# Optimization experiments

Measured on AMD Instinct MI355X. Metric: run time of the kernel, lower is better.

## Reference

```python
import jax, jax.numpy as jnp
import numpy as np
from jax import lax

EPS = 1e-5

def bn(x, g, b):
    # training-mode BatchNorm2d over (N, H, W)
    m = jnp.mean(x, axis=(0, 2, 3), keepdims=True)
    v = jnp.var(x, axis=(0, 2, 3), keepdims=True)
    return (x - m) * lax.rsqrt(v + EPS) * g[None, :, None, None] + b[None, :, None, None]

def conv1x1(x, W):
    # x: [b,c,h,w], W: [o,c]
    return jnp.einsum('bchw,oc->bohw', x, W)

def conv3x3(x, W):
    # W: [o,i,3,3]
    return lax.conv_general_dilated(x, W, (1, 1), 'SAME',
                                    dimension_numbers=('NCHW', 'OIHW', 'NCHW'))

def lga(x, Wqkv, Wproj, g, b):
    # LinearGlobalAttention: O(N) global attention
    bsz, c, h, w = x.shape
    qkv = conv1x1(x, Wqkv)                       # [b, 3c, h, w]
    q, k, v = jnp.split(qkv, 3, axis=1)
    q = q.reshape(bsz, c, h * w)                 # [b, c, N]
    k = jax.nn.softmax(k.reshape(bsz, c, h * w), axis=-1)
    v = v.reshape(bsz, c, h * w)
    ctx = jnp.einsum('bcn,bdn->bcd', k, v)       # [b, c, c]
    out = jnp.einsum('bcd,bcn->bdn', ctx, q)     # context^T @ q -> [b, c, N]
    out = out.reshape(bsz, c, h, w)
    return jax.nn.relu(bn(conv1x1(out, Wproj), g, b))


def setup_inputs() -> dict:
    key = jax.random.key(0)
    ks = jax.random.split(key, 12)
    B, Cin, Cout, H, W = 16, 128, 256, 64, 64
    wd = Cout // 4  # branch width = 64
    sc = 0.05
    inp = {
        'x': jax.random.normal(ks[0], (B, Cin, H, W), jnp.float32),
        'W_sc': jax.random.normal(ks[1], (Cout, Cin), jnp.float32) * sc,
        'g_sc': jnp.ones((Cout,), jnp.float32),
        'b_sc': jnp.zeros((Cout,), jnp.float32),
        'W1': jax.random.normal(ks[2], (Cout, Cin), jnp.float32) * sc,
        'g1': jnp.ones((Cout,), jnp.float32),
        'b1': jnp.zeros((Cout,), jnp.float32),
        'Wb0': jax.random.normal(ks[3], (wd, wd), jnp.float32) * sc,
        'gb0': jnp.ones((wd,), jnp.float32),
        'bb0': jnp.zeros((wd,), jnp.float32),
        'Wb1': jax.random.normal(ks[4], (wd, wd, 3, 3), jnp.float32) * sc,
        'gb1': jnp.ones((wd,), jnp.float32),
        'bb1': jnp.zeros((wd,), jnp.float32),
        'Wqkv2': jax.random.normal(ks[5], (3 * wd, wd), jnp.float32) * sc,
        'Wproj2': jax.random.normal(ks[6], (wd, wd), jnp.float32) * sc,
        'ga2': jnp.ones((wd,), jnp.float32),
        'ba2': jnp.zeros((wd,), jnp.float32),
        'Wqkv3': jax.random.normal(ks[7], (3 * wd, wd), jnp.float32) * sc,
        'Wproj3': jax.random.normal(ks[8], (wd, wd), jnp.float32) * sc,
        'ga3': jnp.ones((wd,), jnp.float32),
        'ba3': jnp.zeros((wd,), jnp.float32),
        'W2': jax.random.normal(ks[9], (Cout, Cout), jnp.float32) * sc,
        'g2': jnp.ones((Cout,), jnp.float32),
        'b2': jnp.zeros((Cout,), jnp.float32),
    }
    return inp


def reference(x, W_sc, g_sc, b_sc, W1, g1, b1,
              Wb0, gb0, bb0, Wb1, gb1, bb1,
              Wqkv2, Wproj2, ga2, ba2,
              Wqkv3, Wproj3, ga3, ba3,
              W2, g2, b2):
    residual = bn(conv1x1(x, W_sc), g_sc, b_sc)
    h = jax.nn.relu(bn(conv1x1(x, W1), g1, b1))      # [b, 256, H, W]
    s0, s1, s2, s3 = jnp.split(h, 4, axis=1)          # width = 64 each
    o0 = jax.nn.relu(bn(conv1x1(s0, Wb0), gb0, bb0))  # k=1 branch
    o1 = jax.nn.relu(bn(conv3x3(s1, Wb1), gb1, bb1))  # k=3 branch
    o2 = lga(s2, Wqkv2, Wproj2, ga2, ba2)             # k=5 -> attention
    o3 = lga(s3, Wqkv3, Wproj3, ga3, ba3)             # k=7 -> attention
    out = jnp.concatenate([o0, o1, o2, o3], axis=1)
    out = bn(conv1x1(out, W2), g2, b2) + residual
    return jax.nn.relu(out)
```

## Files before the change

### kernel.cpp

```cpp
#include <hip/hip_runtime.h>
#include <hip/hip_bf16.h>

using bf16 = __hip_bfloat16;
typedef __bf16 bf16v8 __attribute__((ext_vector_type(8)));
typedef float f32x4 __attribute__((ext_vector_type(4)));

#define HW 4096
#define ROWS 65536
#define BRSTRIDE 4194304

#define AS1 const __attribute__((address_space(1))) void*
#define AS3 __attribute__((address_space(3))) void*

__global__ void r4_cvt_w(const float* __restrict__ Wsc, const float* __restrict__ W1,
                         const float* __restrict__ Wb0,
                         const float* __restrict__ Wqkv2, const float* __restrict__ Wqkv3,
                         const float* __restrict__ W2, const float* __restrict__ Wb1,
                         bf16* __restrict__ wbase, bf16* __restrict__ wp,
                         float* __restrict__ stats) {
    int i = blockIdx.x * 256 + threadIdx.x;
    if (i < 2048) stats[i] = 0.f;
    if (i < 159744) {
        const float* s; int off;
        if      (i < 32768)  { s = Wsc;   off = i; }
        else if (i < 65536)  { s = W1;    off = i - 32768; }
        else if (i < 69632)  { s = Wb0;   off = i - 65536; }
        else if (i < 81920)  { s = Wqkv2; off = i - 69632; }
        else if (i < 94208)  { s = Wqkv3; off = i - 81920; }
        else                 { s = W2;    off = i - 94208; }
        wbase[i] = __float2bfloat16(s[off]);
    } else {
        int k = i - 159744;
        int tap = k / 4096, rem = k % 4096;
        int o = rem >> 6, c = rem & 63;
        wp[k] = __float2bfloat16(Wb1[(size_t)(o * 64 + c) * 9 + tap]);
    }
}

__global__ void r4_cvt_x(const float* __restrict__ x, bf16* __restrict__ xT) {
    __shared__ bf16 tile[64 * 65];
    int b = blockIdx.z, c0 = blockIdx.y * 64, n0 = blockIdx.x * 64;
    int t = threadIdx.x;
#pragma unroll
    for (int i = 0; i < 4; i++) {
        int idx = i * 256 + t;
        int cc = idx >> 4, n4 = (idx & 15) * 4;
        float4 v = *(const float4*)&x[((size_t)(b * 128 + c0 + cc)) * HW + n0 + n4];
        tile[(n4 + 0) * 65 + cc] = __float2bfloat16(v.x);
        tile[(n4 + 1) * 65 + cc] = __float2bfloat16(v.y);
        tile[(n4 + 2) * 65 + cc] = __float2bfloat16(v.z);
        tile[(n4 + 3) * 65 + cc] = __float2bfloat16(v.w);
    }
    __syncthreads();
#pragma unroll
    for (int i = 0; i < 2; i++) {
        int u = i * 256 + t;
        int nn = u >> 3, p = u & 7;
        bf16v8 v;
#pragma unroll
        for (int j = 0; j < 8; j++) v[j] = (__bf16)tile[nn * 65 + p * 8 + j];
        *(bf16v8*)&xT[((size_t)(b * HW + n0 + nn)) * 128 + c0 + p * 8] = v;
    }
}

template <int KK>
__global__ __launch_bounds__(256) void ga_gemm(
        const bf16* __restrict__ A, int a_stride,
        const bf16* __restrict__ W, int w_stride,
        bf16* __restrict__ out0, bf16* __restrict__ out1, int split,
        int out_stride,
        float* __restrict__ stat0, float* __restrict__ stat1,
        int scol0, int scol1,
        const float* __restrict__ tsums,
        const float* __restrict__ tg0, const float* __restrict__ tb0,
        const float* __restrict__ tg1, const float* __restrict__ tb1,
        const float* __restrict__ tg2, const float* __restrict__ tb2,
        const float* __restrict__ tg3, const float* __restrict__ tb3) {
    __shared__ bf16 shmem[2 * 128 * 128];
    __shared__ float sredS[256], sredQ[256];
    __shared__ float scS[256], shS[256];
    bf16* As = shmem;
    bf16* Ws = shmem + 16384;

    int t = threadIdx.x;
    int wave = t >> 6, lane = t & 63;
    int lo = lane & 15, quad = lane >> 4;
    int wr = wave >> 1, wc = wave & 1;
    int b = blockIdx.z;
    long grow = (long)b * HW + blockIdx.x * 128;
    int o0 = blockIdx.y * 128;
    const bf16* Wb = W + (long)o0 * w_stride;

    if (tsums) {
        int qi = t >> 6, ci = t & 63;
        const float* gp = qi == 0 ? tg0 : qi == 1 ? tg1 : qi == 2 ? tg2 : tg3;
        const float* bp = qi == 0 ? tb0 : qi == 1 ? tb1 : qi == 2 ? tb2 : tb3;
        float mean = tsums[t] * (1.f / 65536.f);
        float var  = tsums[256 + t] * (1.f / 65536.f) - mean * mean;
        float s = gp[ci] * rsqrtf(var + 1e-5f);
        scS[t] = s; shS[t] = bp[ci] - mean * s;
    }

    f32x4 acc[4][4];
#pragma unroll
    for (int m = 0; m < 4; m++)
#pragma unroll
        for (int n = 0; n < 4; n++) acc[m][n] = (f32x4){0.f, 0.f, 0.f, 0.f};

#pragma unroll
    for (int ph = 0; ph < KK / 128; ph++) {
        int k0 = ph * 128;
#pragma unroll
        for (int j = 0; j < 8; j++) {
            int i = j * 4 + wave;
            int ci = i * 64 + lane;
            int R = ci >> 4, cc = ci & 15;
            int sw = ((cc ^ (R & 7)) << 3);
            __builtin_amdgcn_global_load_lds(
                (AS1)(A + (grow + R) * (long)a_stride + k0 + sw),
                (AS3)(As + i * 512), 16, 0, 0);
            __builtin_amdgcn_global_load_lds(
                (AS1)(Wb + (long)R * w_stride + k0 + sw),
                (AS3)(Ws + i * 512), 16, 0, 0);
        }
        asm volatile("s_waitcnt vmcnt(0)" ::: "memory");
        __syncthreads();
        if (tsums) {
#pragma unroll
            for (int i = 0; i < 8; i++) {
                int ci = i * 256 + t;
                int R = ci >> 4, p = ci & 15;
                int chb = k0 + ((p ^ (R & 7)) << 3);
                bf16v8 v = *(const bf16v8*)&As[R * 128 + p * 8];
#pragma unroll
                for (int j = 0; j < 8; j++) {
                    float f = (float)v[j] * scS[chb + j] + shS[chb + j];
                    v[j] = (__bf16)fmaxf(f, 0.f);
                }
                *(bf16v8*)&As[R * 128 + p * 8] = v;
            }
            __syncthreads();
        }
#pragma unroll
        for (int ks = 0; ks < 128; ks += 32) {
            int kk = (ks >> 3) + quad;
            bf16v8 av[4], wv[4];
#pragma unroll
            for (int m = 0; m < 4; m++) {
                int R = wr * 64 + m * 16 + lo;
                av[m] = *(const bf16v8*)&As[R * 128 + ((kk ^ (R & 7)) << 3)];
            }
#pragma unroll
            for (int n = 0; n < 4; n++) {
                int R = wc * 64 + n * 16 + lo;
                wv[n] = *(const bf16v8*)&Ws[R * 128 + ((kk ^ (R & 7)) << 3)];
            }
#pragma unroll
            for (int m = 0; m < 4; m++)
#pragma unroll
                for (int n = 0; n < 4; n++)
                    acc[m][n] = __builtin_amdgcn_mfma_f32_16x16x32_bf16(av[m], wv[n], acc[m][n], 0, 0, 0);
        }
        __syncthreads();
    }

    bf16* Ot = shmem;
#pragma unroll
    for (int m = 0; m < 4; m++)
#pragma unroll
        for (int n = 0; n < 4; n++)
#pragma unroll
            for (int r = 0; r < 4; r++)
                Ot[(wr * 64 + m * 16 + quad * 4 + r) * 136 + wc * 64 + n * 16 + lo] =
                    __float2bfloat16(acc[m][n][r]);
    __syncthreads();
    bool low = o0 < split;
    bf16* op = low ? out0 : out1;
    int oc0 = low ? o0 : o0 - split;
#pragma unroll
    for (int i = 0; i < 8; i++) {
        int u = i * 256 + t;
        int lr = u >> 4, cg = u & 15;
        *(bf16v8*)&op[(grow + lr) * (long)out_stride + oc0 + cg * 8] =
            *(const bf16v8*)&Ot[lr * 136 + cg * 8];
    }
    if (stat0) {
        int c = t & 127, half = t >> 7;
        float s = 0.f, q = 0.f;
#pragma unroll
        for (int r = 0; r < 64; r++) {
            float v = __bfloat162float(Ot[(half * 64 + r) * 136 + c]);
            s += v; q += v * v;
        }
        sredS[t] = s; sredQ[t] = q;
        __syncthreads();
        if (t < 128) {
            float ss = sredS[t] + sredS[t + 128];
            float qq = sredQ[t] + sredQ[t + 128];
            float* st = low ? stat0 : stat1;
            int ci = (low ? scol0 + o0 : scol1 + o0 - split) + c;
            atomicAdd(&st[ci], ss);
            atomicAdd(&st[256 + ci], qq);
        }
    }
}

__global__ __launch_bounds__(256) void gq_gemm(
        const bf16* __restrict__ y1,
        const bf16* __restrict__ wq2, const bf16* __restrict__ wq3,
        const bf16* __restrict__ wb0,
        bf16* __restrict__ qs, bf16* __restrict__ ks, bf16* __restrict__ vs,
        bf16* __restrict__ obuf, float* __restrict__ stats,
        const float* __restrict__ asums,
        const float* __restrict__ g1, const float* __restrict__ b1) {
    __shared__ bf16 shmem[256 * 64 + 64 * 64];
    __shared__ float sredS[256], sredQ[256];
    __shared__ float scS[64], shS[64];
    bf16* As = shmem;
    bf16* Ws = shmem + 256 * 64;

    int t = threadIdx.x;
    int wave = t >> 6, lane = t & 63;
    int lo = lane & 15, quad = lane >> 4;
    int b = blockIdx.z, y = blockIdx.y;
    long grow = (long)b * HW + blockIdx.x * 256;

    const bf16* Ab; const bf16* Wb; bf16* outp; int ostride; float* st; int col0;
    if (y == 6) {
        Ab = y1; Wb = wb0; outp = obuf; ostride = 256; st = stats; col0 = 0;
    } else {
        int br = y / 3, sel = y - br * 3;
        col0 = 128 + br * 64;
        Ab = y1 + col0;
        Wb = (br ? wq3 : wq2) + sel * 4096;
        outp = (sel == 0 ? qs : sel == 1 ? ks : vs) + (long)br * BRSTRIDE;
        ostride = 64; st = nullptr;
    }
    if (t < 64) {
        int ch = col0 + t;
        float mean = asums[ch] * (1.f / 65536.f);
        float var  = asums[256 + ch] * (1.f / 65536.f) - mean * mean;
        float s = g1[ch] * rsqrtf(var + 1e-5f);
        scS[t] = s; shS[t] = b1[ch] - mean * s;
    }

    f32x4 acc[4][4];
#pragma unroll
    for (int m = 0; m < 4; m++)
#pragma unroll
        for (int n = 0; n < 4; n++) acc[m][n] = (f32x4){0.f, 0.f, 0.f, 0.f};

#pragma unroll
    for (int j = 0; j < 8; j++) {
        int ci = (j * 4 + wave) * 64 + lane;
        int R = ci >> 3, cc = ci & 7;
        __builtin_amdgcn_global_load_lds(
            (AS1)(Ab + (grow + R) * 256L + ((cc ^ (R & 7)) << 3)),
            (AS3)(As + (j * 4 + wave) * 512), 16, 0, 0);
    }
#pragma unroll
    for (int j = 0; j < 2; j++) {
        int ci = (j * 4 + wave) * 64 + lane;
        int R = ci >> 3, cc = ci & 7;
        __builtin_amdgcn_global_load_lds(
            (AS1)(Wb + R * 64 + ((cc ^ (R & 7)) << 3)),
            (AS3)(Ws + (j * 4 + wave) * 512), 16, 0, 0);
    }
    asm volatile("s_waitcnt vmcnt(0)" ::: "memory");
    __syncthreads();
#pragma unroll
    for (int i = 0; i < 8; i++) {
        int ci = i * 256 + t;
        int R = ci >> 3, p = ci & 7;
        int chb = (p ^ (R & 7)) << 3;
        bf16v8 v = *(const bf16v8*)&As[R * 64 + p * 8];
#pragma unroll
        for (int j = 0; j < 8; j++) {
            float f = (float)v[j] * scS[chb + j] + shS[chb + j];
            v[j] = (__bf16)fmaxf(f, 0.f);
        }
        *(bf16v8*)&As[R * 64 + p * 8] = v;
    }
    __syncthreads();

#pragma unroll
    for (int ks_ = 0; ks_ < 64; ks_ += 32) {
        bf16v8 av[4], wv[4];
#pragma unroll
        for (int m = 0; m < 4; m++) {
            int R = wave * 64 + m * 16 + lo;
            av[m] = *(const bf16v8*)&As[R * 64 + ((((ks_ >> 3) + quad) ^ (R & 7)) << 3)];
        }
#pragma unroll
        for (int n = 0; n < 4; n++) {
            int o = n * 16 + lo;
            wv[n] = *(const bf16v8*)&Ws[o * 64 + ((((ks_ >> 3) + quad) ^ (o & 7)) << 3)];
        }
#pragma unroll
        for (int m = 0; m < 4; m++)
#pragma unroll
            for (int n = 0; n < 4; n++)
                acc[m][n] = __builtin_amdgcn_mfma_f32_16x16x32_bf16(av[m], wv[n], acc[m][n], 0, 0, 0);
    }
    __syncthreads();

    bf16* Ot = shmem;
#pragma unroll
    for (int m = 0; m < 4; m++)
#pragma unroll
        for (int n = 0; n < 4; n++)
#pragma unroll
            for (int r = 0; r < 4; r++)
                Ot[(wave * 64 + m * 16 + quad * 4 + r) * 72 + n * 16 + lo] =
                    __float2bfloat16(acc[m][n][r]);
    __syncthreads();
#pragma unroll
    for (int i = 0; i < 8; i++) {
        int u = i * 256 + t;
        int lr = u >> 3, cg = u & 7;
        *(bf16v8*)&outp[(grow + lr) * (long)ostride + cg * 8] =
            *(const bf16v8*)&Ot[lr * 72 + cg * 8];
    }
    if (st) {
        int c = t & 63, qtr = t >> 6;
        float s = 0.f, q = 0.f;
#pragma unroll
        for (int r = 0; r < 64; r++) {
            float v = __bfloat162float(Ot[(qtr * 64 + r) * 72 + c]);
            s += v; q += v * v;
        }
        sredS[t] = s; sredQ[t] = q;
        __syncthreads();
        if (t < 64) {
            float ss = sredS[t] + sredS[t + 64] + sredS[t + 128] + sredS[t + 192];
            float qq = sredQ[t] + sredQ[t + 64] + sredQ[t + 128] + sredQ[t + 192];
            atomicAdd(&st[t], ss);
            atomicAdd(&st[256 + t], qq);
        }
    }
}

__global__ __launch_bounds__(256) void gp_gemm(
        const bf16* __restrict__ qs, const bf16* __restrict__ M,
        bf16* __restrict__ obuf, float* __restrict__ stats) {
    __shared__ bf16 shmem[256 * 64 + 64 * 64];
    __shared__ float sredS[256], sredQ[256];
    bf16* As = shmem;
    bf16* Ws = shmem + 256 * 64;

    int t = threadIdx.x;
    int wave = t >> 6, lane = t & 63;
    int lo = lane & 15, quad = lane >> 4;
    int b = blockIdx.z, y = blockIdx.y;
    long grow = (long)b * HW + blockIdx.x * 256;
    const bf16* Ab = qs + (long)y * BRSTRIDE;
    const bf16* Wb = M + y * 65536 + (long)b * 4096;
    int oc0 = 128 + y * 64;

    f32x4 acc[4][4];
#pragma unroll
    for (int m = 0; m < 4; m++)
#pragma unroll
        for (int n = 0; n < 4; n++) acc[m][n] = (f32x4){0.f, 0.f, 0.f, 0.f};

#pragma unroll
    for (int j = 0; j < 8; j++) {
        int ci = (j * 4 + wave) * 64 + lane;
        int R = ci >> 3, cc = ci & 7;
        __builtin_amdgcn_global_load_lds(
            (AS1)(Ab + (grow + R) * 64L + ((cc ^ (R & 7)) << 3)),
            (AS3)(As + (j * 4 + wave) * 512), 16, 0, 0);
    }
#pragma unroll
    for (int j = 0; j < 2; j++) {
        int ci = (j * 4 + wave) * 64 + lane;
        int R = ci >> 3, cc = ci & 7;
        __builtin_amdgcn_global_load_lds(
            (AS1)(Wb + R * 64 + ((cc ^ (R & 7)) << 3)),
            (AS3)(Ws + (j * 4 + wave) * 512), 16, 0, 0);
    }
    asm volatile("s_waitcnt vmcnt(0)" ::: "memory");
    __syncthreads();

#pragma unroll
    for (int ks_ = 0; ks_ < 64; ks_ += 32) {
        bf16v8 av[4], wv[4];
#pragma unroll
        for (int m = 0; m < 4; m++) {
            int R = wave * 64 + m * 16 + lo;
            av[m] = *(const bf16v8*)&As[R * 64 + ((((ks_ >> 3) + quad) ^ (R & 7)) << 3)];
        }
#pragma unroll
        for (int n = 0; n < 4; n++) {
            int o = n * 16 + lo;
            wv[n] = *(const bf16v8*)&Ws[o * 64 + ((((ks_ >> 3) + quad) ^ (o & 7)) << 3)];
        }
#pragma unroll
        for (int m = 0; m < 4; m++)
#pragma unroll
            for (int n = 0; n < 4; n++)
                acc[m][n] = __builtin_amdgcn_mfma_f32_16x16x32_bf16(av[m], wv[n], acc[m][n], 0, 0, 0);
    }
    __syncthreads();

    bf16* Ot = shmem;
#pragma unroll
    for (int m = 0; m < 4; m++)
#pragma unroll
        for (int n = 0; n < 4; n++)
#pragma unroll
            for (int r = 0; r < 4; r++)
                Ot[(wave * 64 + m * 16 + quad * 4 + r) * 72 + n * 16 + lo] =
                    __float2bfloat16(acc[m][n][r]);
    __syncthreads();
#pragma unroll
    for (int i = 0; i < 8; i++) {
        int u = i * 256 + t;
        int lr = u >> 3, cg = u & 7;
        *(bf16v8*)&obuf[(grow + lr) * 256L + oc0 + cg * 8] =
            *(const bf16v8*)&Ot[lr * 72 + cg * 8];
    }
    {
        int c = t & 63, qtr = t >> 6;
        float s = 0.f, q = 0.f;
#pragma unroll
        for (int r = 0; r < 64; r++) {
            float v = __bfloat162float(Ot[(qtr * 64 + r) * 72 + c]);
            s += v; q += v * v;
        }
        sredS[t] = s; sredQ[t] = q;
        __syncthreads();
        if (t < 64) {
            float ss = sredS[t] + sredS[t + 64] + sredS[t + 128] + sredS[t + 192];
            float qq = sredQ[t] + sredQ[t + 64] + sredQ[t + 128] + sredQ[t + 192];
            atomicAdd(&stats[oc0 + t], ss);
            atomicAdd(&stats[256 + oc0 + t], qq);
        }
    }
}

__global__ __launch_bounds__(256) void r12_conv3(
        const bf16* __restrict__ hT, const bf16* __restrict__ wp,
        bf16* __restrict__ obuf, float* __restrict__ stat,
        const float* __restrict__ asums,
        const float* __restrict__ g1, const float* __restrict__ b1) {
    __shared__ bf16 As[6 * 66 * 64];
    __shared__ bf16 Wt[9 * 64 * 64];
    __shared__ float sredS[256], sredQ[256];
    __shared__ float scS[64], shS[64];

    int t = threadIdx.x;
    int wave = t >> 6, lane = t & 63;
    int lo = lane & 15, quad = lane >> 4;
    int b = blockIdx.y, y0 = blockIdx.x * 4;

    if (t < 64) {
        int ch = 64 + t;
        float mean = asums[ch] * (1.f / 65536.f);
        float var  = asums[256 + ch] * (1.f / 65536.f) - mean * mean;
        float s = g1[ch] * rsqrtf(var + 1e-5f);
        scS[t] = s; shS[t] = b1[ch] - mean * s;
    }

#pragma unroll
    for (int j = 0; j < 18; j++) {
        int i = j * 4 + wave;
        int ci = i * 64 + lane;
        int tap = ci >> 9, rem = ci & 511, o = rem >> 3, ck = rem & 7;
        __builtin_amdgcn_global_load_lds(
            (AS1)(wp + tap * 4096 + o * 64 + ((ck ^ (o & 7)) << 3)),
            (AS3)(Wt + i * 512), 16, 0, 0);
    }
#pragma unroll
    for (int j = 0; j < 12; j++) {
        int i = j * 4 + wave;
        int row = i >> 3, seg = i & 7;
        int yy = y0 - 1 + row;
        if (yy >= 0 && yy < 64) {
            int xg = seg * 8 + (lane >> 3), ck = lane & 7;
            __builtin_amdgcn_global_load_lds(
                (AS1)(hT + ((long)b * HW + yy * 64 + xg) * 256 + 64 + ((ck ^ (xg & 7)) << 3)),
                (AS3)(As + row * 4224 + 64 + seg * 512), 16, 0, 0);
        } else {
            *(bf16v8*)&As[row * 4224 + 64 + seg * 512 + lane * 8] = (bf16v8){0,0,0,0,0,0,0,0};
        }
    }
    if (t < 96) {
        int yr = t >> 4, side = (t >> 3) & 1, ck = t & 7;
        *(bf16v8*)&As[yr * 4224 + (side ? 65 : 0) * 64 + ck * 8] = (bf16v8){0,0,0,0,0,0,0,0};
    }
    asm volatile("s_waitcnt vmcnt(0)" ::: "memory");
    __syncthreads();
#pragma unroll
    for (int i = 0; i < 12; i++) {
        int ci = i * 256 + t;
        int row = ci >> 9, rem = ci & 511;
        int xg = rem >> 3, p = rem & 7;
        int yy = y0 - 1 + row;
        if (yy >= 0 && yy < 64) {
            int chb = (p ^ (xg & 7)) << 3;
            bf16v8 v = *(const bf16v8*)&As[row * 4224 + (xg + 1) * 64 + p * 8];
#pragma unroll
            for (int j = 0; j < 8; j++) {
                float f = (float)v[j] * scS[chb + j] + shS[chb + j];
                v[j] = (__bf16)fmaxf(f, 0.f);
            }
            *(bf16v8*)&As[row * 4224 + (xg + 1) * 64 + p * 8] = v;
        }
    }
    __syncthreads();

    f32x4 acc[4][4];
#pragma unroll
    for (int m = 0; m < 4; m++)
#pragma unroll
        for (int n = 0; n < 4; n++) acc[m][n] = (f32x4){0.f, 0.f, 0.f, 0.f};

#pragma unroll
    for (int tap = 0; tap < 9; tap++) {
        int dy = tap / 3 - 1, dx = tap % 3 - 1;
        int yr = wave + 1 + dy;
#pragma unroll
        for (int ks8 = 0; ks8 < 8; ks8 += 4) {
            int kk = ks8 + quad;
            bf16v8 wv[4];
#pragma unroll
            for (int ot = 0; ot < 4; ot++) {
                int o = ot * 16 + lo;
                wv[ot] = *(const bf16v8*)&Wt[tap * 4096 + o * 64 + ((kk ^ (o & 7)) << 3)];
            }
#pragma unroll
            for (int m = 0; m < 4; m++) {
                int xp = m * 16 + lo + dx;
                bf16v8 av = *(const bf16v8*)&As[yr * 4224 + (xp + 1) * 64 + ((kk ^ (xp & 7)) << 3)];
#pragma unroll
                for (int ot = 0; ot < 4; ot++)
                    acc[m][ot] = __builtin_amdgcn_mfma_f32_16x16x32_bf16(av, wv[ot], acc[m][ot], 0, 0, 0);
            }
        }
    }
    __syncthreads();

    bf16* Ot = As;
#pragma unroll
    for (int m = 0; m < 4; m++)
#pragma unroll
        for (int ot = 0; ot < 4; ot++)
#pragma unroll
            for (int r = 0; r < 4; r++)
                Ot[(wave * 64 + m * 16 + quad * 4 + r) * 72 + ot * 16 + lo] =
                    __float2bfloat16(acc[m][ot][r]);
    __syncthreads();

    long grow = (long)b * HW + y0 * 64;
#pragma unroll
    for (int i = 0; i < 8; i++) {
        int u = i * 256 + t;
        int lr = u >> 3, cg = u & 7;
        *(bf16v8*)&obuf[(grow + lr) * 256 + 64 + cg * 8] = *(const bf16v8*)&Ot[lr * 72 + cg * 8];
    }
    {
        int c = t & 63, qtr = t >> 6;
        float s = 0.f, q = 0.f;
#pragma unroll
        for (int r = 0; r < 64; r++) {
            float v = __bfloat162float(Ot[(qtr * 64 + r) * 72 + c]);
            s += v; q += v * v;
        }
        sredS[t] = s; sredQ[t] = q;
        __syncthreads();
        if (t < 64) {
            float ss = sredS[t] + sredS[t + 64] + sredS[t + 128] + sredS[t + 192];
            float qq = sredQ[t] + sredQ[t + 64] + sredQ[t + 128] + sredQ[t + 192];
            atomicAdd(&stat[64 + t], ss);
            atomicAdd(&stat[256 + 64 + t], qq);
        }
    }
}

__global__ __launch_bounds__(256) void r14_softctx(
        const bf16* __restrict__ ks_t, const bf16* __restrict__ vs_t,
        float* __restrict__ ctx_p, float* __restrict__ lpart) {
    __shared__ bf16 Ks[64 * 136];
    __shared__ bf16 Vs[64 * 136];
    __shared__ float red[32 * 64];
    int t = threadIdx.x;
    int wave = t >> 6, lane = t & 63;
    int lo = lane & 15, quad = lane >> 4;
    int b = blockIdx.y, bx = blockIdx.x, z = blockIdx.z;
    const bf16* kb = ks_t + (long)z * BRSTRIDE;
    const bf16* vb = vs_t + (long)z * BRSTRIDE;

    f32x4 acc[4];
#pragma unroll
    for (int ot = 0; ot < 4; ot++) acc[ot] = (f32x4){0.f, 0.f, 0.f, 0.f};
    float sm[8];
#pragma unroll
    for (int j = 0; j < 8; j++) sm[j] = 0.f;

    for (int it = 0; it < 2; it++) {
        long n0 = ((long)bx * 2 + it) * 128;
        __syncthreads();
#pragma unroll
        for (int sub = 0; sub < 4; sub++) {
            int r = sub * 32 + (t >> 3), cg = t & 7;
            long row = (long)b * HW + n0 + r;
            bf16v8 k8 = *(const bf16v8*)(kb + row * 64 + cg * 8);
            bf16v8 v8 = *(const bf16v8*)(vb + row * 64 + cg * 8);
#pragma unroll
            for (int j = 0; j < 8; j++) {
                int c = cg * 8 + j;
                float e = expf((float)k8[j]);
                sm[j] += e;
                Ks[c * 136 + r] = __float2bfloat16(e);
                Vs[c * 136 + r] = (bf16)v8[j];
            }
        }
        __syncthreads();
#pragma unroll
        for (int ks = 0; ks < 128; ks += 32) {
            bf16v8 av = *(const bf16v8*)&Ks[(wave * 16 + lo) * 136 + ks + quad * 8];
#pragma unroll
            for (int ot = 0; ot < 4; ot++) {
                bf16v8 bv = *(const bf16v8*)&Vs[(ot * 16 + lo) * 136 + ks + quad * 8];
                acc[ot] = __builtin_amdgcn_mfma_f32_16x16x32_bf16(av, bv, acc[ot], 0, 0, 0);
            }
        }
    }
    long blk = ((long)z * 16 + b) * 16 + bx;
#pragma unroll
    for (int ot = 0; ot < 4; ot++) {
#pragma unroll
        for (int r = 0; r < 4; r++) {
            int c = wave * 16 + quad * 4 + r;
            int d = ot * 16 + lo;
            ctx_p[(blk * 64 + c) * 64 + d] = acc[ot][r];
        }
    }
    {
        int rg = t >> 3, cg = t & 7;
#pragma unroll
        for (int j = 0; j < 8; j++) red[rg * 64 + cg * 8 + j] = sm[j];
        __syncthreads();
        if (t < 64) {
            float s = 0.f;
#pragma unroll
            for (int i = 0; i < 32; i++) s += red[i * 64 + t];
            lpart[blk * 64 + t] = s;
        }
    }
}

__global__ __launch_bounds__(256) void r15_mproj(
        const float* __restrict__ Wp2, const float* __restrict__ Wp3,
        const float* __restrict__ ctx_p, const float* __restrict__ lpart,
        bf16* __restrict__ M) {
    __shared__ float ctxS[16 * 68];
    __shared__ float ilS[16];
    int b = blockIdx.x, qq = blockIdx.y, z = blockIdx.z, t = threadIdx.x;
    int e = t & 63, cg = t >> 6;
    const float* Wp = z ? Wp3 : Wp2;
    long zb = (long)z * 16 + b;
#pragma unroll
    for (int i = 0; i < 4; i++) {
        int u = i * 256 + t;
        int c_l = u >> 6, d = u & 63;
        float s = 0.f;
#pragma unroll
        for (int p = 0; p < 16; p++)
            s += ctx_p[((zb * 16 + p) * 64 + qq * 16 + c_l) * 64 + d];
        ctxS[c_l * 68 + d] = s;
    }
    if (t < 16) {
        float l = 0.f;
#pragma unroll
        for (int p = 0; p < 16; p++)
            l += lpart[(zb * 16 + p) * 64 + qq * 16 + t];
        ilS[t] = 1.f / l;
    }
    float wreg[64];
#pragma unroll
    for (int i = 0; i < 16; i++) {
        float4 v = *(const float4*)&Wp[e * 64 + i * 4];
        wreg[i * 4 + 0] = v.x; wreg[i * 4 + 1] = v.y;
        wreg[i * 4 + 2] = v.z; wreg[i * 4 + 3] = v.w;
    }
    __syncthreads();
#pragma unroll
    for (int ci = 0; ci < 4; ci++) {
        int c_l = cg * 4 + ci;
        float a = 0.f;
#pragma unroll
        for (int dg = 0; dg < 16; dg++) {
            float4 cv = *(const float4*)&ctxS[c_l * 68 + dg * 4];
            a += wreg[dg * 4 + 0] * cv.x + wreg[dg * 4 + 1] * cv.y
               + wreg[dg * 4 + 2] * cv.z + wreg[dg * 4 + 3] * cv.w;
        }
        M[(long)z * 65536 + (long)b * 4096 + e * 64 + qq * 16 + c_l] =
            __float2bfloat16(a * ilS[c_l]);
    }
}

__global__ void r6_final(const bf16* __restrict__ y2, const bf16* __restrict__ ysc,
                         const float* __restrict__ s2sums, const float* __restrict__ scsums,
                         const float* __restrict__ g2, const float* __restrict__ b2,
                         const float* __restrict__ gsc, const float* __restrict__ bsc,
                         float* __restrict__ out) {
    __shared__ float lo_[64 * 65];
    __shared__ float sc2[64], sh2[64], scc[64], shc[64];
    int b = blockIdx.z, c0 = blockIdx.y * 64, n0 = blockIdx.x * 64;
    int t = threadIdx.x;
    if (t < 64) {
        int ch = c0 + t;
        float m2 = s2sums[ch] * (1.f / 65536.f);
        float v2 = s2sums[256 + ch] * (1.f / 65536.f) - m2 * m2;
        float s = g2[ch] * rsqrtf(v2 + 1e-5f);
        sc2[t] = s; sh2[t] = b2[ch] - m2 * s;
        float mc = scsums[ch] * (1.f / 65536.f);
        float vc = scsums[256 + ch] * (1.f / 65536.f) - mc * mc;
        float s2_ = gsc[ch] * rsqrtf(vc + 1e-5f);
        scc[t] = s2_; shc[t] = bsc[ch] - mc * s2_;
    }
    __syncthreads();
    for (int half = 0; half < 2; half++) {
        int r = half * 32 + (t >> 3), cc = (t & 7) * 8;
        long row = (long)b * HW + n0 + r;
        bf16v8 a8 = *(const bf16v8*)&y2[row * 256 + c0 + cc];
        bf16v8 s8 = *(const bf16v8*)&ysc[row * 256 + c0 + cc];
#pragma unroll
        for (int j = 0; j < 8; j++) {
            int c = cc + j;
            float v = (float)a8[j] * sc2[c] + sh2[c] + (float)s8[j] * scc[c] + shc[c];
            lo_[c * 65 + r] = fmaxf(v, 0.f);
        }
    }
    __syncthreads();
#pragma unroll
    for (int i = 0; i < 4; i++) {
        int idx = i * 256 + t;
        int c = idx >> 4, r4 = (idx & 15) * 4;
        float4 w;
        w.x = lo_[c * 65 + r4 + 0];
        w.y = lo_[c * 65 + r4 + 1];
        w.z = lo_[c * 65 + r4 + 2];
        w.w = lo_[c * 65 + r4 + 3];
        *(float4*)&out[((long)(b * 256 + c0 + c)) * HW + n0 + r4] = w;
    }
}

extern "C" void kernel_launch(void* const* d_in, const int* in_sizes, int n_in,
                              void* d_out, int out_size, void* d_ws, size_t ws_size,
                              hipStream_t stream) {
    const float* x     = (const float*)d_in[0];
    const float* Wsc   = (const float*)d_in[1];
    const float* gsc   = (const float*)d_in[2];
    const float* bsc   = (const float*)d_in[3];
    const float* W1    = (const float*)d_in[4];
    const float* g1    = (const float*)d_in[5];
    const float* b1    = (const float*)d_in[6];
    const float* Wb0   = (const float*)d_in[7];
    const float* gb0   = (const float*)d_in[8];
    const float* bb0   = (const float*)d_in[9];
    const float* Wb1   = (const float*)d_in[10];
    const float* gb1   = (const float*)d_in[11];
    const float* bb1   = (const float*)d_in[12];
    const float* Wqkv2 = (const float*)d_in[13];
    const float* Wproj2= (const float*)d_in[14];
    const float* ga2   = (const float*)d_in[15];
    const float* ba2   = (const float*)d_in[16];
    const float* Wqkv3 = (const float*)d_in[17];
    const float* Wproj3= (const float*)d_in[18];
    const float* ga3   = (const float*)d_in[19];
    const float* ba3   = (const float*)d_in[20];
    const float* W2    = (const float*)d_in[21];
    const float* g2    = (const float*)d_in[22];
    const float* b2    = (const float*)d_in[23];

    char* ws = (char*)d_ws;
    float* stats = (float*)ws;
    bf16*  M     = (bf16*)(ws + 32768);
    bf16*  wbase = (bf16*)(ws + 294912);
    bf16*  wsc_b = wbase;
    bf16*  wb0_b = wbase + 65536;
    bf16*  wq2_b = wbase + 69632;
    bf16*  wq3_b = wbase + 81920;
    bf16*  w2_b  = wbase + 94208;
    bf16*  wb1p  = (bf16*)(ws + 614400);
    bf16*  xT    = (bf16*)(ws + 1048576);
    bf16*  vs    = (bf16*)(ws + 1048576);
    bf16*  ysc   = (bf16*)(ws + 17825792);
    bf16*  y1    = (bf16*)(ws + 51380224);
    float* ctx_p = (float*)(ws + 51380224);
    float* lpart = (float*)(ws + 51380224 + 8388608);
    bf16*  y2    = y1;
    bf16*  obuf  = (bf16*)d_out;
    bf16*  qs    = (bf16*)((char*)d_out + 33554432);
    bf16*  ks    = (bf16*)((char*)d_out + 50331648);

    r4_cvt_w<<<dim3(768), 256, 0, stream>>>(Wsc, W1, Wb0, Wqkv2, Wqkv3, W2, Wb1,
                                            wbase, wb1p, stats);
    r4_cvt_x<<<dim3(64, 2, 16), 256, 0, stream>>>(x, xT);

    ga_gemm<128><<<dim3(32, 4, 16), 256, 0, stream>>>(
        xT, 128, wsc_b, 128,
        ysc, y1, 256, 256, stats, stats + 512, 0, 0,
        nullptr, nullptr, nullptr, nullptr, nullptr, nullptr, nullptr, nullptr, nullptr);

    r12_conv3<<<dim3(16, 16), 256, 0, stream>>>(y1, wb1p, obuf, stats + 1024,
                                                stats + 512, g1, b1);
    gq_gemm<<<dim3(16, 7, 16), 256, 0, stream>>>(
        y1, wq2_b, wq3_b, wb0_b, qs, ks, vs, obuf, stats + 1024,
        stats + 512, g1, b1);

    r14_softctx<<<dim3(16, 16, 2), 256, 0, stream>>>(ks, vs, ctx_p, lpart);
    r15_mproj<<<dim3(16, 4, 2), 256, 0, stream>>>(Wproj2, Wproj3, ctx_p, lpart, M);
    gp_gemm<<<dim3(16, 2, 16), 256, 0, stream>>>(qs, M, obuf, stats + 1024);

    ga_gemm<256><<<dim3(32, 2, 16), 256, 0, stream>>>(
        obuf, 256, w2_b, 256,
        y2, y2, 1 << 28, 256, stats + 1536, stats + 1536, 0, 0,
        stats + 1024, gb0, bb0, gb1, bb1, ga2, ba2, ga3, ba3);

    r6_final<<<dim3(64, 4, 16), 256, 0, stream>>>(y2, ysc, stats + 1536, stats + 0,
                                                  g2, b2, gsc, bsc, (float*)d_out);
}
```

Baseline: 281.8 us.

## Fuse input transpose/convert into first GEMM, reuse A tile across output blocks

The separate fp32→bf16 transpose kernel is removed. The first GEMM now reads x directly, converts and transposes it into swizzled LDS, then loops over all four 128-wide output blocks while keeping the A tile resident. BN statistics are reduced from fp32 accumulators with wave shuffles instead of re-reading the bf16 output tile. This cuts the xT round-trip through global memory and one launch, at the cost of a serialized output loop per block and fewer blocks (512) in flight.

Measured after the change: 282.3 us. About the same (+0.2%).

```diff
diff --git a/kernel.cpp b/kernel.cpp
--- a/kernel.cpp
+++ b/kernel.cpp
@@ -37,110 +37,59 @@
     }
 }
 
-__global__ void r4_cvt_x(const float* __restrict__ x, bf16* __restrict__ xT) {
-    __shared__ bf16 tile[64 * 65];
-    int b = blockIdx.z, c0 = blockIdx.y * 64, n0 = blockIdx.x * 64;
-    int t = threadIdx.x;
-#pragma unroll
-    for (int i = 0; i < 4; i++) {
-        int idx = i * 256 + t;
-        int cc = idx >> 4, n4 = (idx & 15) * 4;
-        float4 v = *(const float4*)&x[((size_t)(b * 128 + c0 + cc)) * HW + n0 + n4];
-        tile[(n4 + 0) * 65 + cc] = __float2bfloat16(v.x);
-        tile[(n4 + 1) * 65 + cc] = __float2bfloat16(v.y);
-        tile[(n4 + 2) * 65 + cc] = __float2bfloat16(v.z);
-        tile[(n4 + 3) * 65 + cc] = __float2bfloat16(v.w);
-    }
-    __syncthreads();
-#pragma unroll
-    for (int i = 0; i < 2; i++) {
-        int u = i * 256 + t;
-        int nn = u >> 3, p = u & 7;
-        bf16v8 v;
-#pragma unroll
-        for (int j = 0; j < 8; j++) v[j] = (__bf16)tile[nn * 65 + p * 8 + j];
-        *(bf16v8*)&xT[((size_t)(b * HW + n0 + nn)) * 128 + c0 + p * 8] = v;
-    }
-}
-
-template <int KK>
-__global__ __launch_bounds__(256) void ga_gemm(
-        const bf16* __restrict__ A, int a_stride,
-        const bf16* __restrict__ W, int w_stride,
-        bf16* __restrict__ out0, bf16* __restrict__ out1, int split,
-        int out_stride,
-        float* __restrict__ stat0, float* __restrict__ stat1,
-        int scol0, int scol1,
-        const float* __restrict__ tsums,
-        const float* __restrict__ tg0, const float* __restrict__ tb0,
-        const float* __restrict__ tg1, const float* __restrict__ tb1,
-        const float* __restrict__ tg2, const float* __restrict__ tb2,
-        const float* __restrict__ tg3, const float* __restrict__ tb3) {
-    __shared__ bf16 shmem[2 * 128 * 128];
-    __shared__ float sredS[256], sredQ[256];
-    __shared__ float scS[256], shS[256];
-    bf16* As = shmem;
-    bf16* Ws = shmem + 16384;
+__global__ __launch_bounds__(256) void gx_gemm(
+        const float* __restrict__ x, const bf16* __restrict__ W,
+        bf16* __restrict__ ysc, bf16* __restrict__ y1,
+        float* __restrict__ stats) {
+    __shared__ bf16 As[128 * 128];
+    __shared__ bf16 Ws[128 * 128];
+    __shared__ float sredS[4 * 128], sredQ[4 * 128];
 
     int t = threadIdx.x;
     int wave = t >> 6, lane = t & 63;
     int lo = lane & 15, quad = lane >> 4;
     int wr = wave >> 1, wc = wave & 1;
-    int b = blockIdx.z;
-    long grow = (long)b * HW + blockIdx.x * 128;
-    int o0 = blockIdx.y * 128;
-    const bf16* Wb = W + (long)o0 * w_stride;
-
-    if (tsums) {
-        int qi = t >> 6, ci = t & 63;
-        const float* gp = qi == 0 ? tg0 : qi == 1 ? tg1 : qi == 2 ? tg2 : tg3;
-        const float* bp = qi == 0 ? tb0 : qi == 1 ? tb1 : qi == 2 ? tb2 : tb3;
-        float mean = tsums[t] * (1.f / 65536.f);
-        float var  = tsums[256 + t] * (1.f / 65536.f) - mean * mean;
-        float s = gp[ci] * rsqrtf(var + 1e-5f);
-        scS[t] = s; shS[t] = bp[ci] - mean * s;
-    }
-
-    f32x4 acc[4][4];
-#pragma unroll
-    for (int m = 0; m < 4; m++)
-#pragma unroll
-        for (int n = 0; n < 4; n++) acc[m][n] = (f32x4){0.f, 0.f, 0.f, 0.f};
-
-#pragma unroll
-    for (int ph = 0; ph < KK / 128; ph++) {
-        int k0 = ph * 128;
+    int b = blockIdx.y;
+    long n0 = (long)blockIdx.x * 128;
+    long grow = (long)b * HW + n0;
+
+    {
+        int ch = t >> 1, half = t & 1;
+        const float* xrow = x + ((size_t)(b * 128 + ch)) * HW + n0 + half * 64;
+#pragma unroll
+        for (int i = 0; i < 16; i++) {
+            float4 v = *(const float4*)&xrow[i * 4];
+#pragma unroll
+            for (int j = 0; j < 4; j++) {
+                int R = half * 64 + i * 4 + j;
+                float f = (j == 0) ? v.x : (j == 1) ? v.y : (j == 2) ? v.z : v.w;
+                As[R * 128 + ((((ch >> 3) ^ (R & 7)) << 3) | (ch & 7))] =
+                    __float2bfloat16(f);
+            }
+        }
+    }
+    __syncthreads();
+
+    for (int y = 0; y < 4; y++) {
+        int o0 = y * 128;
+        const bf16* Wb = W + (long)o0 * 128;
 #pragma unroll
         for (int j = 0; j < 8; j++) {
             int i = j * 4 + wave;
             int ci = i * 64 + lane;
             int R = ci >> 4, cc = ci & 15;
-            int sw = ((cc ^ (R & 7)) << 3);
             __builtin_amdgcn_global_load_lds(
-                (AS1)(A + (grow + R) * (long)a_stride + k0 + sw),
-                (AS3)(As + i * 512), 16, 0, 0);
-            __builtin_amdgcn_global_load_lds(
-                (AS1)(Wb + (long)R * w_stride + k0 + sw),
+                (AS1)(Wb + R * 128 + ((cc ^ (R & 7)) << 3)),
                 (AS3)(Ws + i * 512), 16, 0, 0);
         }
         asm volatile("s_waitcnt vmcnt(0)" ::: "memory");
         __syncthreads();
-        if (tsums) {
-#pragma unroll
-            for (int i = 0; i < 8; i++) {
-                int ci = i * 256 + t;
-                int R = ci >> 4, p = ci & 15;
-                int chb = k0 + ((p ^ (R & 7)) << 3);
-                bf16v8 v = *(const bf16v8*)&As[R * 128 + p * 8];
-#pragma unroll
-                for (int j = 0; j < 8; j++) {
-                    float f = (float)v[j] * scS[chb + j] + shS[chb + j];
-                    v[j] = (__bf16)fmaxf(f, 0.f);
-                }
-                *(bf16v8*)&As[R * 128 + p * 8] = v;
-            }
-            __syncthreads();
-        }
+
+        f32x4 acc[4][4];
+#pragma unroll
+        for (int m = 0; m < 4; m++)
+#pragma unroll
+            for (int n = 0; n < 4; n++) acc[m][n] = (f32x4){0.f, 0.f, 0.f, 0.f};
 #pragma unroll
         for (int ks = 0; ks < 128; ks += 32) {
             int kk = (ks >> 3) + quad;
@@ -162,46 +111,65 @@
                     acc[m][n] = __builtin_amdgcn_mfma_f32_16x16x32_bf16(av[m], wv[n], acc[m][n], 0, 0, 0);
         }
         __syncthreads();
-    }
-
-    bf16* Ot = shmem;
-#pragma unroll
-    for (int m = 0; m < 4; m++)
-#pragma unroll
-        for (int n = 0; n < 4; n++)
-#pragma unroll
-            for (int r = 0; r < 4; r++)
-                Ot[(wr * 64 + m * 16 + quad * 4 + r) * 136 + wc * 64 + n * 16 + lo] =
-                    __float2bfloat16(acc[m][n][r]);
-    __syncthreads();
-    bool low = o0 < split;
-    bf16* op = low ? out0 : out1;
-    int oc0 = low ? o0 : o0 - split;
-#pragma unroll
-    for (int i = 0; i < 8; i++) {
-        int u = i * 256 + t;
-        int lr = u >> 4, cg = u & 15;
-        *(bf16v8*)&op[(grow + lr) * (long)out_stride + oc0 + cg * 8] =
-            *(const bf16v8*)&Ot[lr * 136 + cg * 8];
-    }
-    if (stat0) {
-        int c = t & 127, half = t >> 7;
-        float s = 0.f, q = 0.f;
-#pragma unroll
-        for (int r = 0; r < 64; r++) {
-            float v = __bfloat162float(Ot[(half * 64 + r) * 136 + c]);
-            s += v; q += v * v;
-        }
-        sredS[t] = s; sredQ[t] = q;
-        __syncthreads();
+
+        {
+            float cS[4], cQ[4];
+#pragma unroll
+            for (int n = 0; n < 4; n++) {
+                float s = 0.f, q = 0.f;
+#pragma unroll
+                for (int m = 0; m < 4; m++)
+#pragma unroll
+                    for (int r = 0; r < 4; r++) {
+                        float v = acc[m][n][r];
+                        s += v; q += v * v;
+                    }
+                cS[n] = s; cQ[n] = q;
+            }
+#pragma unroll
+            for (int n = 0; n < 4; n++) {
+                cS[n] += __shfl_xor(cS[n], 16); cS[n] += __shfl_xor(cS[n], 32);
+                cQ[n] += __shfl_xor(cQ[n], 16); cQ[n] += __shfl_xor(cQ[n], 32);
+            }
+            if (lane < 16) {
+#pragma unroll
+                for (int n = 0; n < 4; n++) {
+                    sredS[wave * 128 + wc * 64 + n * 16 + lane] = cS[n];
+                    sredQ[wave * 128 + wc * 64 + n * 16 + lane] = cQ[n];
+                }
+            }
+        }
+        bf16* Ot = Ws;
+#pragma unroll
+        for (int m = 0; m < 4; m++)
+#pragma unroll
+            for (int n = 0; n < 4; n++)
+#pragma unroll
+                for (int r = 0; r < 4; r++)
+                    Ot[(wr * 64 + m * 16 + quad * 4 + r) * 128 + wc * 64 + n * 16 + lo] =
+                        __float2bfloat16(acc[m][n][r]);
+        __syncthreads();
+
+        bool low = o0 < 256;
+        bf16* op = low ? ysc : y1;
+        int oc0 = low ? o0 : o0 - 256;
+#pragma unroll
+        for (int i = 0; i < 8; i++) {
+            int u = i * 256 + t;
+            int lr = u >> 4, cg = u & 15;
+            *(bf16v8*)&op[(grow + lr) * 256L + oc0 + cg * 8] =
+                *(const bf16v8*)&Ot[lr * 128 + cg * 8];
+        }
         if (t < 128) {
-            float ss = sredS[t] + sredS[t + 128];
-            float qq = sredQ[t] + sredQ[t + 128];
-            float* st = low ? stat0 : stat1;
-            int ci = (low ? scol0 + o0 : scol1 + o0 - split) + c;
+            int c = t, g = c >> 6;
+            float ss = sredS[g * 128 + c] + sredS[(2 + g) * 128 + c];
+            float qq = sredQ[g * 128 + c] + sredQ[(2 + g) * 128 + c];
+            float* st = low ? stats : stats + 512;
+            int ci = oc0 + c;
             atomicAdd(&st[ci], ss);
             atomicAdd(&st[256 + ci], qq);
         }
+        __syncthreads();
     }
 }
 
@@ -786,7 +754,6 @@
     bf16*  wq3_b = wbase + 81920;
     bf16*  w2_b  = wbase + 94208;
     bf16*  wb1p  = (bf16*)(ws + 614400);
-    bf16*  xT    = (bf16*)(ws + 1048576);
     bf16*  vs    = (bf16*)(ws + 1048576);
     bf16*  ysc   = (bf16*)(ws + 17825792);
     bf16*  y1    = (bf16*)(ws + 51380224);
@@ -799,12 +766,8 @@
 
     r4_cvt_w<<<dim3(768), 256, 0, stream>>>(Wsc, W1, Wb0, Wqkv2, Wqkv3, W2, Wb1,
                                             wbase, wb1p, stats);
-    r4_cvt_x<<<dim3(64, 2, 16), 256, 0, stream>>>(x, xT);
-
-    ga_gemm<128><<<dim3(32, 4, 16), 256, 0, stream>>>(
-        xT, 128, wsc_b, 128,
-        ysc, y1, 256, 256, stats, stats + 512, 0, 0,
-        nullptr, nullptr, nullptr, nullptr, nullptr, nullptr, nullptr, nullptr, nullptr);
+
+    gx_gemm<<<dim3(32, 16), 256, 0, stream>>>(x, wsc_b, ysc, y1, stats);
 
     r12_conv3<<<dim3(16, 16), 256, 0, stream>>>(y1, wb1p, obuf, stats + 1024,
                                                 stats + 512, g1, b1);
@@ -816,11 +779,147 @@
     r15_mproj<<<dim3(16, 4, 2), 256, 0, stream>>>(Wproj2, Wproj3, ctx_p, lpart, M);
     gp_gemm<<<dim3(16, 2, 16), 256, 0, stream>>>(qs, M, obuf, stats + 1024);
 
-    ga_gemm<256><<<dim3(32, 2, 16), 256, 0, stream>>>(
-        obuf, 256, w2_b, 256,
-        y2, y2, 1 << 28, 256, stats + 1536, stats + 1536, 0, 0,
+    {
+    }
+    extern __global__ void ga2_gemm(const bf16*, const bf16*, bf16*, float*,
+                                    const float*, const float*, const float*,
+                                    const float*, const float*, const float*,
+                                    const float*, const float*, const float*);
+    ga2_gemm<<<dim3(32, 2, 16), 256, 0, stream>>>(
+        obuf, w2_b, y2, stats + 1536,
         stats + 1024, gb0, bb0, gb1, bb1, ga2, ba2, ga3, ba3);
 
     r6_final<<<dim3(64, 4, 16), 256, 0, stream>>>(y2, ysc, stats + 1536, stats + 0,
                                                   g2, b2, gsc, bsc, (float*)d_out);
 }
+
+__global__ __launch_bounds__(256) void ga2_gemm(
+        const bf16* __restrict__ A, const bf16* __restrict__ W,
+        bf16* __restrict__ out0, float* __restrict__ stat0,
+        const float* __restrict__ tsums,
+        const float* __restrict__ tg0, const float* __restrict__ tb0,
+        const float* __restrict__ tg1, const float* __restrict__ tb1,
+        const float* __restrict__ tg2, const float* __restrict__ tb2,
+        const float* __restrict__ tg3, const float* __restrict__ tb3) {
+    __shared__ bf16 shmem[2 * 128 * 128];
+    __shared__ float sredS[256], sredQ[256];
+    __shared__ float scS[256], shS[256];
+    bf16* As = shmem;
+    bf16* Ws = shmem + 16384;
+
+    int t = threadIdx.x;
+    int wave = t >> 6, lane = t & 63;
+    int lo = lane & 15, quad = lane >> 4;
+    int wr = wave >> 1, wc = wave & 1;
+    int b = blockIdx.z;
+    long grow = (long)b * HW + blockIdx.x * 128;
+    int o0 = blockIdx.y * 128;
+    const bf16* Wb = W + (long)o0 * 256;
+
+    {
+        int qi = t >> 6, ci = t & 63;
+        const float* gp = qi == 0 ? tg0 : qi == 1 ? tg1 : qi == 2 ? tg2 : tg3;
+        const float* bp = qi == 0 ? tb0 : qi == 1 ? tb1 : qi == 2 ? tb2 : tb3;
+        float mean = tsums[t] * (1.f / 65536.f);
+        float var  = tsums[256 + t] * (1.f / 65536.f) - mean * mean;
+        float s = gp[ci] * rsqrtf(var + 1e-5f);
+        scS[t] = s; shS[t] = bp[ci] - mean * s;
+    }
+
+    f32x4 acc[4][4];
+#pragma unroll
+    for (int m = 0; m < 4; m++)
+#pragma unroll
+        for (int n = 0; n < 4; n++) acc[m][n] = (f32x4){0.f, 0.f, 0.f, 0.f};
+
+#pragma unroll
+    for (int ph = 0; ph < 2; ph++) {
+        int k0 = ph * 128;
+#pragma unroll
+        for (int j = 0; j < 8; j++) {
+            int i = j * 4 + wave;
+            int ci = i * 64 + lane;
+            int R = ci >> 4, cc = ci & 15;
+            int sw = ((cc ^ (R & 7)) << 3);
+            __builtin_amdgcn_global_load_lds(
+                (AS1)(A + (grow + R) * 256L + k0 + sw),
+                (AS3)(As + i * 512), 16, 0, 0);
+            __builtin_amdgcn_global_load_lds(
+                (AS1)(Wb + (long)R * 256 + k0 + sw),
+                (AS3)(Ws + i * 512), 16, 0, 0);
+        }
+        asm volatile("s_waitcnt vmcnt(0)" ::: "memory");
+        __syncthreads();
+#pragma unroll
+        for (int i = 0; i < 8; i++) {
+            int ci = i * 256 + t;
+            int R = ci >> 4, p = ci & 15;
+            int chb = k0 + ((p ^ (R & 7)) << 3);
+            bf16v8 v = *(const bf16v8*)&As[R * 128 + p * 8];
+#pragma unroll
+            for (int j = 0; j < 8; j++) {
+                float f = (float)v[j] * scS[chb + j] + shS[chb + j];
+                v[j] = (__bf16)fmaxf(f, 0.f);
+            }
+            *(bf16v8*)&As[R * 128 + p * 8] = v;
+        }
+        __syncthreads();
+#pragma unroll
+        for (int ks = 0; ks < 128; ks += 32) {
+            int kk = (ks >> 3) + quad;
+            bf16v8 av[4], wv[4];
+#pragma unroll
+            for (int m = 0; m < 4; m++) {
+                int R = wr * 64 + m * 16 + lo;
+                av[m] = *(const bf16v8*)&As[R * 128 + ((kk ^ (R & 7)) << 3)];
+            }
+#pragma unroll
+            for (int n = 0; n < 4; n++) {
+                int R = wc * 64 + n * 16 + lo;
+                wv[n] = *(const bf16v8*)&Ws[R * 128 + ((kk ^ (R & 7)) << 3)];
+            }
+#pragma unroll
+            for (int m = 0; m < 4; m++)
+#pragma unroll
+                for (int n = 0; n < 4; n++)
+                    acc[m][n] = __builtin_amdgcn_mfma_f32_16x16x32_bf16(av[m], wv[n], acc[m][n], 0, 0, 0);
+        }
+        __syncthreads();
+    }
+
+    bf16* Ot = shmem;
+#pragma unroll
+    for (int m = 0; m < 4; m++)
+#pragma unroll
+        for (int n = 0; n < 4; n++)
+#pragma unroll
+            for (int r = 0; r < 4; r++)
+                Ot[(wr * 64 + m * 16 + quad * 4 + r) * 136 + wc * 64 + n * 16 + lo] =
+                    __float2bfloat16(acc[m][n][r]);
+    __syncthreads();
+#pragma unroll
+    for (int i = 0; i < 8; i++) {
+        int u = i * 256 + t;
+        int lr = u >> 4, cg = u & 15;
+        *(bf16v8*)&out0[(grow + lr) * 256L + o0 + cg * 8] =
+            *(const bf16v8*)&Ot[lr * 136 + cg * 8];
+    }
+    {
+        int c = t & 127, half = t >> 7;
+        float s = 0.f, q = 0.f;
+#pragma unroll
+        for (int r = 0; r < 64; r++) {
+            float v = __bfloat162float(Ot[(half * 64 + r) * 136 + c]);
+            s += v; q += v * v;
+        }
+        sredS[t] = s; sredQ[t] = q;
+        __syncthreads();
+        if (t < 128) {
+            float ss = sredS[t] + sredS[t + 128];
+            float qq = sredQ[t] + sredQ[t + 128];
+            int ci = o0 + c;
+            atomicAdd(&stat0[ci], ss);
+            atomicAdd(&stat0[256 + ci], qq);
+        }
+    }
+}
```
